# Kernel optimization log

Hardware: AMD Instinct MI355X
Metric: run time of the kernel (lower is better)

The kernel has to match this reference:

```python
import jax, jax.numpy as jnp
import numpy as np

EPS = 1e-6

def _rms_norm(x):
    xf = x.astype(jnp.float32)
    var = jnp.mean(xf * xf, axis=-1, keepdims=True)
    return (xf * jax.lax.rsqrt(var + EPS)).astype(x.dtype)

def setup_inputs() -> dict:
    key = jax.random.key(0)
    k1, k2 = jax.random.split(key)
    B, N, T, D = 16, 768, 48, 2048
    patches = jax.random.normal(k1, (B, N, D), dtype=jnp.float32)
    task_tokens = jax.random.normal(k2, (B, T, D), dtype=jnp.float32)
    task_token_mask = jnp.ones((B, T), dtype=bool)  # True = valid token
    return {"patches": patches, "task_tokens": task_tokens, "task_token_mask": task_token_mask}

def reference(patches, task_tokens, task_token_mask):
    D = patches.shape[-1]
    scale = 1.0 / np.sqrt(D)
    patches_n = _rms_norm(patches)          # [B,N,D]
    task_n = _rms_norm(task_tokens)         # [B,T,D]
    # additive attention bias: 0 for valid task tokens, finfo.min for masked
    neg = jnp.finfo(patches_n.dtype).min
    bias = jnp.where(task_token_mask[:, None, :], 0.0, neg).astype(patches_n.dtype)  # [B,1,T]
    # scaled dot-product attention: patches attend to task tokens
    logits = jnp.einsum('bnd,btd->bnt', patches_n, task_n) * scale + bias
    attn = jax.nn.softmax(logits, axis=-1)
    queries_raw = jnp.einsum('bnt,btd->bnd', attn, task_n)  # [B,N,D]
    queries = _rms_norm(queries_raw)
    # importance score: each query scores every patch
    score = jnp.einsum('bnd,bmd->bnm', queries, patches_n) * scale  # [B,N,N]
    # differentiable selection (select_soft, noise_scale=None):
    # straight-through: hard one-hot of argmax + soft softmax - stop_grad(soft)
    soft = jax.nn.softmax(score, axis=-1)
    hard = jax.nn.one_hot(jnp.argmax(score, axis=-1), score.shape[-1], dtype=score.dtype)
    sel = hard + soft - jax.lax.stop_gradient(soft)
    return sel
```

## Files before the change

kernel.cpp:

```cpp
#include <hip/hip_runtime.h>
#include <math.h>

#define NB 16
#define NN 768
#define NT 48
#define ND 2048
#define NROW (NB*NN)
#define SCALE 0.02209708691207961f
#define NEGBIG (-3.4028234663852886e38f)
#define TAU 2e-3f
#define KS 512
#define MSPLIT 16
#define MCH (NN/MSPLIT)

typedef _Float16 f16;
typedef f16  f16x8 __attribute__((ext_vector_type(8)));
typedef f16  f16x4 __attribute__((ext_vector_type(4)));
typedef float f32x4 __attribute__((ext_vector_type(4)));

__device__ __forceinline__ void stage16(const void* g, void* l) {
    __builtin_amdgcn_global_load_lds(
        (const __attribute__((address_space(1))) unsigned int*)g,
        (__attribute__((address_space(3))) unsigned int*)l, 16, 0, 0);
}

__device__ __forceinline__ void ins4m(float v[4], int idx[4], float nv, int ni) {
    const bool b0 = (v[0] >= nv);
    const bool b1 = (v[1] >= nv);
    const bool b2 = (v[2] >= nv);
    const bool b3 = (v[3] >= nv);
    const int pos = (int)b0 + (int)b1 + (int)b2 + (int)b3;
    if (pos <= 3) { if (pos == 3) { v[3] = nv; idx[3] = ni; } else { v[3] = v[2]; idx[3] = idx[2]; } }
    if (pos <= 2) { if (pos == 2) { v[2] = nv; idx[2] = ni; } else { v[2] = v[1]; idx[2] = idx[1]; } }
    if (pos <= 1) { if (pos == 1) { v[1] = nv; idx[1] = ni; } else { v[1] = v[0]; idx[1] = idx[0]; } }
    if (pos == 0) { v[0] = nv; idx[0] = ni; }
}

__global__ __launch_bounds__(256) void k_prep_task(const float* __restrict__ task,
                                                   float* __restrict__ task_n,
                                                   f16* __restrict__ t_hi,
                                                   f16* __restrict__ t_lo) {
    __shared__ float sred[8];
    const int row = blockIdx.x;
    const float4* src = (const float4*)(task + (size_t)row * ND);
    const int tid = threadIdx.x;
    float4 v0 = src[tid];
    float4 v1 = src[tid + 256];
    float s = v0.x*v0.x + v0.y*v0.y + v0.z*v0.z + v0.w*v0.w
            + v1.x*v1.x + v1.y*v1.y + v1.z*v1.z + v1.w*v1.w;
    #pragma unroll
    for (int off = 32; off > 0; off >>= 1) s += __shfl_down(s, off, 64);
    if ((tid & 63) == 0) sred[tid >> 6] = s;
    __syncthreads();
    if (tid == 0)
        sred[4] = 1.0f / sqrtf((sred[0]+sred[1]+sred[2]+sred[3]) * (1.0f/ND) + 1e-6f);
    __syncthreads();
    const float inv = sred[4];
    const size_t o = (size_t)row * ND;
    f16x4 h0, l0, h1, l1;
    float4 n0, n1;
    #pragma unroll
    for (int e = 0; e < 4; e++) {
        float f0 = (&v0.x)[e] * inv, f1 = (&v1.x)[e] * inv;
        (&n0.x)[e] = f0; (&n1.x)[e] = f1;
        f16 a = (f16)f0; h0[e] = a; l0[e] = (f16)(f0 - (float)a);
        f16 c = (f16)f1; h1[e] = c; l1[e] = (f16)(f1 - (float)c);
    }
    *(float4*)&task_n[o + tid*4]          = n0;
    *(float4*)&task_n[o + (tid+256)*4]    = n1;
    *(f16x4*)&t_hi[o + tid*4]             = h0;
    *(f16x4*)&t_lo[o + tid*4]             = l0;
    *(f16x4*)&t_hi[o + (tid+256)*4]       = h1;
    *(f16x4*)&t_lo[o + (tid+256)*4]       = l1;
}

__global__ __launch_bounds__(256) void k_R(const float* __restrict__ patches,
                                           const f16* __restrict__ t_hi,
                                           const f16* __restrict__ t_lo,
                                           float* __restrict__ Rpart,
                                           float* __restrict__ ssqpart) {
    __shared__ __align__(16) char Ah[64*128], Al[64*128];
    __shared__ __align__(16) char Bh[48*128], Bl[48*128];
    const int rt = blockIdx.x, ks = blockIdx.y, b = blockIdx.z;
    const int tid = threadIdx.x, wid = tid >> 6, lane = tid & 63;
    const int q15 = lane & 15, g4 = lane >> 4;
    const int trow = tid >> 2, tq = tid & 3;
    const int lr = lane >> 3, lgch = (lane & 7) ^ lr;
    const int cxor = q15 & 7;

    const float* gP = patches + ((size_t)(b*NN + rt*64))*ND + ks*KS;
    const f16* gTh = t_hi + (size_t)b*NT*ND + ks*KS;
    const f16* gTl = t_lo + (size_t)b*NT*ND + ks*KS;

    f32x4 acc[3];
    #pragma unroll
    for (int j = 0; j < 3; j++) acc[j] = (f32x4){0.f,0.f,0.f,0.f};
    float ssq = 0.f;

    const float* aptr = gP + (size_t)trow*ND + tq*16;
    float4 va[4], vb[4];
    #pragma unroll
    for (int k = 0; k < 4; k++) va[k] = *(const float4*)(aptr + k*4);

    auto body = [&](float4 (&v)[4], float4 (&vn)[4], int kk, bool last) {
        #pragma unroll
        for (int t2 = 0; t2 < 2; t2++) {
            const int u = wid + 4*t2;
            if (u < 6) {
                stage16(gTh + (size_t)(u*8 + lr)*ND + kk + lgch*8, Bh + u*1024);
                stage16(gTl + (size_t)(u*8 + lr)*ND + kk + lgch*8, Bl + u*1024);
            }
        }
        __builtin_amdgcn_sched_barrier(0);
        if (!last) {
            #pragma unroll
            for (int k = 0; k < 4; k++)
                vn[k] = *(const float4*)(aptr + kk + 64 + k*4);
        }
        __builtin_amdgcn_sched_barrier(0);
        float lssq = 0.f;
        f16x8 hi8[2], lo8[2];
        #pragma unroll
        for (int k = 0; k < 4; k++)
            #pragma unroll
            for (int e = 0; e < 4; e++) {
                const float f = (&v[k].x)[e];
                lssq += f*f;
                const f16 h = (f16)f;
                hi8[k>>1][(k&1)*4 + e] = h;
                lo8[k>>1][(k&1)*4 + e] = (f16)(f - (float)h);
            }
        lssq += __shfl_xor(lssq, 1, 64);
        lssq += __shfl_xor(lssq, 2, 64);
        if (tq == 0) ssq += lssq;
        const int rb = trow * 128;
        #pragma unroll
        for (int c = 0; c < 2; c++) {
            const int ch = (2*tq + c) ^ (trow & 7);
            *(f16x8*)(Ah + rb + ch*16) = hi8[c];
            *(f16x8*)(Al + rb + ch*16) = lo8[c];
        }
        __builtin_amdgcn_sched_barrier(0);
        if (last) asm volatile("s_waitcnt vmcnt(0)" ::: "memory");
        else      asm volatile("s_waitcnt vmcnt(4)" ::: "memory");
        asm volatile("s_waitcnt lgkmcnt(0)" ::: "memory");
        __builtin_amdgcn_s_barrier();
        __builtin_amdgcn_sched_barrier(0);
        #pragma unroll
        for (int ksub = 0; ksub < 2; ksub++) {
            const int chb = ((ksub*4 + g4) ^ cxor) << 4;
            const f16x8 a_h = *(const f16x8*)(Ah + (wid*16 + q15)*128 + chb);
            const f16x8 a_l = *(const f16x8*)(Al + (wid*16 + q15)*128 + chb);
            #pragma unroll
            for (int j = 0; j < 3; j++) {
                const f16x8 b_h = *(const f16x8*)(Bh + (j*16 + q15)*128 + chb);
                const f16x8 b_l = *(const f16x8*)(Bl + (j*16 + q15)*128 + chb);
                acc[j] = __builtin_amdgcn_mfma_f32_16x16x32_f16(a_h, b_h, acc[j], 0, 0, 0);
                acc[j] = __builtin_amdgcn_mfma_f32_16x16x32_f16(a_l, b_h, acc[j], 0, 0, 0);
                acc[j] = __builtin_amdgcn_mfma_f32_16x16x32_f16(a_h, b_l, acc[j], 0, 0, 0);
            }
        }
        asm volatile("" ::: "memory");
        __builtin_amdgcn_s_barrier();
        __builtin_amdgcn_sched_barrier(0);
    };

    body(va, vb,   0, false);
    body(vb, va,  64, false);
    body(va, vb, 128, false);
    body(vb, va, 192, false);
    body(va, vb, 256, false);
    body(vb, va, 320, false);
    body(va, vb, 384, false);
    body(vb, va, 448, true);

    const int grow = b*NN + rt*64;
    #pragma unroll
    for (int j = 0; j < 3; j++)
        #pragma unroll
        for (int r = 0; r < 4; r++)
            Rpart[((size_t)ks*NROW + grow + wid*16 + g4*4 + r)*48 + j*16 + q15] = acc[j][r];
    if (tq == 0)
        ssqpart[(size_t)ks*NROW + grow + trow] = ssq;
}

__global__ __launch_bounds__(256) void k_combine(const float* __restrict__ Rpart,
                                                 const float* __restrict__ ssqpart,
                                                 const int* __restrict__ mask,
                                                 float* __restrict__ R,
                                                 float* __restrict__ w,
                                                 float* __restrict__ pinv) {
    const int r = blockIdx.x * 256 + threadIdx.x;
    const int b = r / NN;
    float ss = 0.f;
    #pragma unroll
    for (int ks = 0; ks < 4; ks++) ss += ssqpart[(size_t)ks*NROW + r];
    const float pv = 1.0f / sqrtf(ss * (1.0f/ND) + 1e-6f);
    pinv[r] = pv;
    float l[48];
    float mx = -INFINITY;
    #pragma unroll
    for (int t4 = 0; t4 < 12; t4++) {
        float4 a = {0.f,0.f,0.f,0.f};
        #pragma unroll
        for (int ks = 0; ks < 4; ks++) {
            const float4 p = *(const float4*)&Rpart[((size_t)ks*NROW + r)*48 + t4*4];
            a.x += p.x; a.y += p.y; a.z += p.z; a.w += p.w;
        }
        *(float4*)&R[(size_t)r*48 + t4*4] = a;
        #pragma unroll
        for (int e = 0; e < 4; e++) {
            const int t = t4*4 + e;
            const float bias = mask[b*NT + t] ? 0.0f : NEGBIG;
            l[t] = (&a.x)[e] * pv * SCALE + bias;
            mx = fmaxf(mx, l[t]);
        }
    }
    float sum = 0.f;
    #pragma unroll
    for (int t = 0; t < 48; t++) { l[t] = expf(l[t] - mx); sum += l[t]; }
    const float inv = 1.0f / sum;
    #pragma unroll
    for (int t4 = 0; t4 < 12; t4++) {
        float4 o;
        #pragma unroll
        for (int e = 0; e < 4; e++) (&o.x)[e] = l[t4*4 + e] * inv;
        *(float4*)&w[(size_t)r*48 + t4*4] = o;
    }
}

__global__ __launch_bounds__(256) void k_scoreW(const float* __restrict__ w,
                                                const float* __restrict__ R,
                                                const float* __restrict__ pinv,
                                                float4* __restrict__ part) {
    __shared__ float Rl[MCH*48];
    __shared__ float pl[MCH];
    const int rt = blockIdx.x, ms = blockIdx.y;
    const int tid = threadIdx.x;
    const int row = rt*256 + tid;
    const int b = row / NN;
    const int m0g = b*NN + ms*MCH;
    for (int u = tid; u < MCH*12; u += 256) {
        const int m = u / 12, t4 = u % 12;
        *(float4*)&Rl[m*48 + t4*4] = *(const float4*)&R[((size_t)(m0g + m))*48 + t4*4];
    }
    if (tid < MCH) pl[tid] = pinv[m0g + tid];
    __syncthreads();
    float4 wr[12];
    #pragma unroll
    for (int t4 = 0; t4 < 12; t4++)
        wr[t4] = *(const float4*)&w[(size_t)row*48 + t4*4];
    float tv[4] = {-INFINITY, -INFINITY, -INFINITY, -INFINITY};
    int   ti[4] = {0x7FFFFFFF, 0x7FFFFFFF, 0x7FFFFFFF, 0x7FFFFFFF};
    #pragma unroll 2
    for (int m = 0; m < MCH; m += 4) {
        float s0 = 0.f, s1 = 0.f, s2 = 0.f, s3 = 0.f;
        #pragma unroll
        for (int t4 = 0; t4 < 12; t4++) {
            const float4 r0 = *(const float4*)&Rl[(m+0)*48 + t4*4];
            const float4 r1 = *(const float4*)&Rl[(m+1)*48 + t4*4];
            const float4 r2 = *(const float4*)&Rl[(m+2)*48 + t4*4];
            const float4 r3 = *(const float4*)&Rl[(m+3)*48 + t4*4];
            const float4 wv = wr[t4];
            s0 = fmaf(wv.x, r0.x, s0); s1 = fmaf(wv.x, r1.x, s1);
            s2 = fmaf(wv.x, r2.x, s2); s3 = fmaf(wv.x, r3.x, s3);
            s0 = fmaf(wv.y, r0.y, s0); s1 = fmaf(wv.y, r1.y, s1);
            s2 = fmaf(wv.y, r2.y, s2); s3 = fmaf(wv.y, r3.y, s3);
            s0 = fmaf(wv.z, r0.z, s0); s1 = fmaf(wv.z, r1.z, s1);
            s2 = fmaf(wv.z, r2.z, s2); s3 = fmaf(wv.z, r3.z, s3);
            s0 = fmaf(wv.w, r0.w, s0); s1 = fmaf(wv.w, r1.w, s1);
            s2 = fmaf(wv.w, r2.w, s2); s3 = fmaf(wv.w, r3.w, s3);
        }
        s0 *= pl[m+0]; s1 *= pl[m+1]; s2 *= pl[m+2]; s3 *= pl[m+3];
        const float gm = fmaxf(fmaxf(s0, s1), fmaxf(s2, s3));
        if (gm >= tv[3]) {
            const int mg = ms*MCH + m;
            ins4m(tv, ti, s0, mg+0);
            ins4m(tv, ti, s1, mg+1);
            ins4m(tv, ti, s2, mg+2);
            ins4m(tv, ti, s3, mg+3);
        }
    }
    part[((size_t)row*MSPLIT + ms)*2]     = make_float4(tv[0], __int_as_float(ti[0]), tv[1], __int_as_float(ti[1]));
    part[((size_t)row*MSPLIT + ms)*2 + 1] = make_float4(tv[2], __int_as_float(ti[2]), tv[3], __int_as_float(ti[3]));
}

__global__ __launch_bounds__(256) void k_final(const float* __restrict__ patches,
                                               const float* __restrict__ task_n,
                                               const float* __restrict__ w,
                                               const float* __restrict__ pinv,
                                               const float4* __restrict__ part,
                                               float* __restrict__ out) {
    __shared__ float qrow[ND];
    __shared__ float wl[48];
    __shared__ int   scand[64];
    __shared__ float swv[4];
    __shared__ int   swi[4];
    __shared__ int   s_idx, s_cnt;
    const int row = blockIdx.x;
    const int b = row / NN;
    const int tid = threadIdx.x, wid = tid >> 6, lane = tid & 63;

    if (wid == 0) {
        const float2 e = ((const float2*)part)[(size_t)row*64 + lane];
        const float myv = e.x;
        const int   myi = __float_as_int(e.y);
        float v = myv; int i = myi;
        #pragma unroll
        for (int off = 1; off <= 32; off <<= 1) {
            const float ov = __shfl_xor(v, off, 64);
            const int   oi = __shfl_xor(i, off, 64);
            if (ov > v || (ov == v && oi < i)) { v = ov; i = oi; }
        }
        const bool in_tau = (myv >= v - TAU);
        const unsigned long long mb  = __ballot(in_tau);
        const unsigned long long mb4 = __ballot(in_tau && ((lane & 3) == 3));
        if (lane == 0) {
            s_idx = i;
            s_cnt = mb4 ? 999 : __popcll(mb);
        }
        if (in_tau) {
            const unsigned long long below = mb & ((lane == 0) ? 0ull : (~0ull >> (64 - lane)));
            scand[__popcll(below)] = myi;
        }
    }
    __syncthreads();
    const int cnt = s_cnt;
    if (cnt > 1) {
        if (tid < 12) *(float4*)&wl[tid*4] = *(const float4*)&w[(size_t)row*48 + tid*4];
        __syncthreads();
        {
            float q[8] = {0.f,0.f,0.f,0.f,0.f,0.f,0.f,0.f};
            for (int t = 0; t < NT; t++) {
                const float wt = wl[t];
                const float* Tn = task_n + ((size_t)(b*NT + t))*ND + tid*8;
                const float4 u0 = *(const float4*)Tn;
                const float4 u1 = *(const float4*)(Tn + 4);
                q[0] = fmaf(wt, u0.x, q[0]); q[1] = fmaf(wt, u0.y, q[1]);
                q[2] = fmaf(wt, u0.z, q[2]); q[3] = fmaf(wt, u0.w, q[3]);
                q[4] = fmaf(wt, u1.x, q[4]); q[5] = fmaf(wt, u1.y, q[5]);
                q[6] = fmaf(wt, u1.z, q[6]); q[7] = fmaf(wt, u1.w, q[7]);
            }
            #pragma unroll
            for (int e2 = 0; e2 < 8; e2++) qrow[tid*8 + e2] = q[e2];
        }
        __syncthreads();
        float bw = -INFINITY; int bi = 0x7FFFFFFF;
        if (cnt != 999) {
            for (int c = wid; c < cnt; c += 4) {
                const int m = scand[c];
                const float* prow = patches + ((size_t)b*NN + m)*ND + lane*32;
                const float* qp = qrow + lane*32;
                float s = 0.f;
                #pragma unroll
                for (int k = 0; k < 8; k++) {
                    const float4 p = *(const float4*)(prow + k*4);
                    const float4 qv = *(const float4*)(qp + k*4);
                    s = fmaf(p.x, qv.x, s); s = fmaf(p.y, qv.y, s);
                    s = fmaf(p.z, qv.z, s); s = fmaf(p.w, qv.w, s);
                }
                #pragma unroll
                for (int off = 32; off > 0; off >>= 1) s += __shfl_down(s, off, 64);
                if (lane == 0) {
                    s *= pinv[b*NN + m];
                    if (s > bw || (s == bw && m < bi)) { bw = s; bi = m; }
                }
            }
        } else {
            for (int m = wid; m < NN; m += 4) {
                const float* prow = patches + ((size_t)b*NN + m)*ND + lane*32;
                const float* qp = qrow + lane*32;
                float s = 0.f;
                #pragma unroll
                for (int k = 0; k < 8; k++) {
                    const float4 p = *(const float4*)(prow + k*4);
                    const float4 qv = *(const float4*)(qp + k*4);
                    s = fmaf(p.x, qv.x, s); s = fmaf(p.y, qv.y, s);
                    s = fmaf(p.z, qv.z, s); s = fmaf(p.w, qv.w, s);
                }
                #pragma unroll
                for (int off = 32; off > 0; off >>= 1) s += __shfl_down(s, off, 64);
                if (lane == 0) {
                    s *= pinv[b*NN + m];
                    if (s > bw || (s == bw && m < bi)) { bw = s; bi = m; }
                }
            }
        }
        if (lane == 0) { swv[wid] = bw; swi[wid] = bi; }
        __syncthreads();
        if (tid == 0) {
            float v = swv[0]; int i = swi[0];
            #pragma unroll
            for (int k = 1; k < 4; k++) {
                if (swv[k] > v || (swv[k] == v && swi[k] < i)) { v = swv[k]; i = swi[k]; }
            }
            s_idx = i;
        }
        __syncthreads();
    }
    const int m = s_idx;
    if (tid < 192) {
        float4 o = {0.f, 0.f, 0.f, 0.f};
        if ((m >> 2) == tid) ((float*)&o)[m & 3] = 1.0f;
        ((float4*)(out + (size_t)row*NN))[tid] = o;
    }
}

extern "C" void kernel_launch(void* const* d_in, const int* in_sizes, int n_in,
                              void* d_out, int out_size, void* d_ws, size_t ws_size,
                              hipStream_t stream) {
    const float* patches = (const float*)d_in[0];
    const float* task    = (const float*)d_in[1];
    const int*   mask    = (const int*)d_in[2];
    float* out = (float*)d_out;

    char* p = (char*)d_ws;
    float* task_n  = (float*)p;  p += (size_t)NB*NT*ND*sizeof(float);
    f16*   t_hi    = (f16*)p;    p += (size_t)NB*NT*ND*sizeof(f16);
    f16*   t_lo    = (f16*)p;    p += (size_t)NB*NT*ND*sizeof(f16);
    float* Rpart   = (float*)p;  p += (size_t)4*NROW*48*sizeof(float);
    float* ssqpart = (float*)p;  p += (size_t)4*NROW*sizeof(float);
    float* R       = (float*)p;  p += (size_t)NROW*48*sizeof(float);
    float* w       = (float*)p;  p += (size_t)NROW*48*sizeof(float);
    float* pinv    = (float*)p;  p += (size_t)NROW*sizeof(float);
    float4* part   = (float4*)p; p += (size_t)NROW*MSPLIT*2*sizeof(float4);

    k_prep_task<<<NB*NT, 256, 0, stream>>>(task, task_n, t_hi, t_lo);
    k_R<<<dim3(NN/64, 4, NB), 256, 0, stream>>>(patches, t_hi, t_lo, Rpart, ssqpart);
    k_combine<<<NROW/256, 256, 0, stream>>>(Rpart, ssqpart, mask, R, w, pinv);
    k_scoreW<<<dim3(NROW/256, MSPLIT), 256, 0, stream>>>(w, R, pinv, part);
    k_final<<<NROW, 256, 0, stream>>>(patches, task_n, w, pinv, part, out);
}
```

Measured before the change: 98.57 us.

## Compute low-rank score matrix with split-f16 MFMA and top-2 candidates

Replaces the scalar FP32 score kernel (w·R with per-thread top-4 insertion) with an MFMA kernel. It uses hi/lo f16 splits of the softmax weights and of the normalized R (three MFMAs per tile), padded to K=64, and keeps top-2 candidates per 64-column chunk via lane shuffles. k_combine now emits the f16 split operands, and k_final reads 24 candidates instead of 64 with a tighter tau. The intent is to move the dominant NxN score work onto matrix cores, at the cost of some precision and fewer candidates for tie detection.

```diff
diff --git a/kernel.cpp b/kernel.cpp
--- a/kernel.cpp
+++ b/kernel.cpp
@@ -8,10 +8,8 @@
 #define NROW (NB*NN)
 #define SCALE 0.02209708691207961f
 #define NEGBIG (-3.4028234663852886e38f)
-#define TAU 2e-3f
+#define TAU 1e-3f
 #define KS 512
-#define MSPLIT 16
-#define MCH (NN/MSPLIT)
 
 typedef _Float16 f16;
 typedef f16  f16x8 __attribute__((ext_vector_type(8)));
@@ -22,18 +20,6 @@
     __builtin_amdgcn_global_load_lds(
         (const __attribute__((address_space(1))) unsigned int*)g,
         (__attribute__((address_space(3))) unsigned int*)l, 16, 0, 0);
-}
-
-__device__ __forceinline__ void ins4m(float v[4], int idx[4], float nv, int ni) {
-    const bool b0 = (v[0] >= nv);
-    const bool b1 = (v[1] >= nv);
-    const bool b2 = (v[2] >= nv);
-    const bool b3 = (v[3] >= nv);
-    const int pos = (int)b0 + (int)b1 + (int)b2 + (int)b3;
-    if (pos <= 3) { if (pos == 3) { v[3] = nv; idx[3] = ni; } else { v[3] = v[2]; idx[3] = idx[2]; } }
-    if (pos <= 2) { if (pos == 2) { v[2] = nv; idx[2] = ni; } else { v[2] = v[1]; idx[2] = idx[1]; } }
-    if (pos <= 1) { if (pos == 1) { v[1] = nv; idx[1] = ni; } else { v[1] = v[0]; idx[1] = idx[0]; } }
-    if (pos == 0) { v[0] = nv; idx[0] = ni; }
 }
 
 __global__ __launch_bounds__(256) void k_prep_task(const float* __restrict__ task,
@@ -187,9 +173,12 @@
 __global__ __launch_bounds__(256) void k_combine(const float* __restrict__ Rpart,
                                                  const float* __restrict__ ssqpart,
                                                  const int* __restrict__ mask,
-                                                 float* __restrict__ R,
                                                  float* __restrict__ w,
-                                                 float* __restrict__ pinv) {
+                                                 float* __restrict__ pinv,
+                                                 f16* __restrict__ Whi,
+                                                 f16* __restrict__ Wlo,
+                                                 f16* __restrict__ Ghi,
+                                                 f16* __restrict__ Glo) {
     const int r = blockIdx.x * 256 + threadIdx.x;
     const int b = r / NN;
     float ss = 0.f;
@@ -207,14 +196,19 @@
             const float4 p = *(const float4*)&Rpart[((size_t)ks*NROW + r)*48 + t4*4];
             a.x += p.x; a.y += p.y; a.z += p.z; a.w += p.w;
         }
-        *(float4*)&R[(size_t)r*48 + t4*4] = a;
+        f16x4 gh, gl;
         #pragma unroll
         for (int e = 0; e < 4; e++) {
+            const float g = (&a.x)[e] * pv;
+            const f16 hh = (f16)g;
+            gh[e] = hh; gl[e] = (f16)(g - (float)hh);
             const int t = t4*4 + e;
             const float bias = mask[b*NT + t] ? 0.0f : NEGBIG;
-            l[t] = (&a.x)[e] * pv * SCALE + bias;
+            l[t] = g * SCALE + bias;
             mx = fmaxf(mx, l[t]);
         }
+        *(f16x4*)&Ghi[(size_t)r*64 + t4*4] = gh;
+        *(f16x4*)&Glo[(size_t)r*64 + t4*4] = gl;
     }
     float sum = 0.f;
     #pragma unroll
@@ -223,66 +217,106 @@
     #pragma unroll
     for (int t4 = 0; t4 < 12; t4++) {
         float4 o;
-        #pragma unroll
-        for (int e = 0; e < 4; e++) (&o.x)[e] = l[t4*4 + e] * inv;
+        f16x4 wh, wlv;
+        #pragma unroll
+        for (int e = 0; e < 4; e++) {
+            const float wv = l[t4*4 + e] * inv;
+            (&o.x)[e] = wv;
+            const f16 hh = (f16)wv;
+            wh[e] = hh; wlv[e] = (f16)(wv - (float)hh);
+        }
         *(float4*)&w[(size_t)r*48 + t4*4] = o;
-    }
-}
-
-__global__ __launch_bounds__(256) void k_scoreW(const float* __restrict__ w,
-                                                const float* __restrict__ R,
-                                                const float* __restrict__ pinv,
+        *(f16x4*)&Whi[(size_t)r*64 + t4*4] = wh;
+        *(f16x4*)&Wlo[(size_t)r*64 + t4*4] = wlv;
+    }
+    const f16x4 z = {(f16)0.f, (f16)0.f, (f16)0.f, (f16)0.f};
+    #pragma unroll
+    for (int t4 = 12; t4 < 16; t4++) {
+        *(f16x4*)&Whi[(size_t)r*64 + t4*4] = z;
+        *(f16x4*)&Wlo[(size_t)r*64 + t4*4] = z;
+        *(f16x4*)&Ghi[(size_t)r*64 + t4*4] = z;
+        *(f16x4*)&Glo[(size_t)r*64 + t4*4] = z;
+    }
+}
+
+__global__ __launch_bounds__(256) void k_scoreM(const f16* __restrict__ Whi,
+                                                const f16* __restrict__ Wlo,
+                                                const f16* __restrict__ Ghi,
+                                                const f16* __restrict__ Glo,
                                                 float4* __restrict__ part) {
-    __shared__ float Rl[MCH*48];
-    __shared__ float pl[MCH];
-    const int rt = blockIdx.x, ms = blockIdx.y;
-    const int tid = threadIdx.x;
-    const int row = rt*256 + tid;
-    const int b = row / NN;
-    const int m0g = b*NN + ms*MCH;
-    for (int u = tid; u < MCH*12; u += 256) {
-        const int m = u / 12, t4 = u % 12;
-        *(float4*)&Rl[m*48 + t4*4] = *(const float4*)&R[((size_t)(m0g + m))*48 + t4*4];
-    }
-    if (tid < MCH) pl[tid] = pinv[m0g + tid];
-    __syncthreads();
-    float4 wr[12];
-    #pragma unroll
-    for (int t4 = 0; t4 < 12; t4++)
-        wr[t4] = *(const float4*)&w[(size_t)row*48 + t4*4];
-    float tv[4] = {-INFINITY, -INFINITY, -INFINITY, -INFINITY};
-    int   ti[4] = {0x7FFFFFFF, 0x7FFFFFFF, 0x7FFFFFFF, 0x7FFFFFFF};
-    #pragma unroll 2
-    for (int m = 0; m < MCH; m += 4) {
-        float s0 = 0.f, s1 = 0.f, s2 = 0.f, s3 = 0.f;
-        #pragma unroll
-        for (int t4 = 0; t4 < 12; t4++) {
-            const float4 r0 = *(const float4*)&Rl[(m+0)*48 + t4*4];
-            const float4 r1 = *(const float4*)&Rl[(m+1)*48 + t4*4];
-            const float4 r2 = *(const float4*)&Rl[(m+2)*48 + t4*4];
-            const float4 r3 = *(const float4*)&Rl[(m+3)*48 + t4*4];
-            const float4 wv = wr[t4];
-            s0 = fmaf(wv.x, r0.x, s0); s1 = fmaf(wv.x, r1.x, s1);
-            s2 = fmaf(wv.x, r2.x, s2); s3 = fmaf(wv.x, r3.x, s3);
-            s0 = fmaf(wv.y, r0.y, s0); s1 = fmaf(wv.y, r1.y, s1);
-            s2 = fmaf(wv.y, r2.y, s2); s3 = fmaf(wv.y, r3.y, s3);
-            s0 = fmaf(wv.z, r0.z, s0); s1 = fmaf(wv.z, r1.z, s1);
-            s2 = fmaf(wv.z, r2.z, s2); s3 = fmaf(wv.z, r3.z, s3);
-            s0 = fmaf(wv.w, r0.w, s0); s1 = fmaf(wv.w, r1.w, s1);
-            s2 = fmaf(wv.w, r2.w, s2); s3 = fmaf(wv.w, r3.w, s3);
-        }
-        s0 *= pl[m+0]; s1 *= pl[m+1]; s2 *= pl[m+2]; s3 *= pl[m+3];
-        const float gm = fmaxf(fmaxf(s0, s1), fmaxf(s2, s3));
-        if (gm >= tv[3]) {
-            const int mg = ms*MCH + m;
-            ins4m(tv, ti, s0, mg+0);
-            ins4m(tv, ti, s1, mg+1);
-            ins4m(tv, ti, s2, mg+2);
-            ins4m(tv, ti, s3, mg+3);
-        }
-    }
-    part[((size_t)row*MSPLIT + ms)*2]     = make_float4(tv[0], __int_as_float(ti[0]), tv[1], __int_as_float(ti[1]));
-    part[((size_t)row*MSPLIT + ms)*2 + 1] = make_float4(tv[2], __int_as_float(ti[2]), tv[3], __int_as_float(ti[3]));
+    const int mt = blockIdx.x, rt = blockIdx.y, b = blockIdx.z;
+    const int tid = threadIdx.x, wid = tid >> 6, lane = tid & 63;
+    const int q15 = lane & 15, g4 = lane >> 4;
+    const int wr = wid >> 1, wc = wid & 1;
+
+    const size_t n0 = (size_t)(b*NN + rt*128 + wr*64);
+    const size_t m0 = (size_t)(b*NN + mt*128 + wc*64);
+    const int mbase = mt*128 + wc*64;
+
+    f16x8 ah[4][2], al[4][2], bh[4][2], bl[4][2];
+    #pragma unroll
+    for (int i = 0; i < 4; i++)
+        #pragma unroll
+        for (int ksub = 0; ksub < 2; ksub++) {
+            const size_t ao = (n0 + i*16 + q15)*64 + ksub*32 + g4*8;
+            ah[i][ksub] = *(const f16x8*)&Whi[ao];
+            al[i][ksub] = *(const f16x8*)&Wlo[ao];
+            const size_t bo = (m0 + i*16 + q15)*64 + ksub*32 + g4*8;
+            bh[i][ksub] = *(const f16x8*)&Ghi[bo];
+            bl[i][ksub] = *(const f16x8*)&Glo[bo];
+        }
+
+    f32x4 acc[4][4];
+    #pragma unroll
+    for (int i = 0; i < 4; i++)
+        #pragma unroll
+        for (int j = 0; j < 4; j++) acc[i][j] = (f32x4){0.f,0.f,0.f,0.f};
+
+    #pragma unroll
+    for (int ksub = 0; ksub < 2; ksub++)
+        #pragma unroll
+        for (int i = 0; i < 4; i++)
+            #pragma unroll
+            for (int j = 0; j < 4; j++) {
+                acc[i][j] = __builtin_amdgcn_mfma_f32_16x16x32_f16(ah[i][ksub], bh[j][ksub], acc[i][j], 0, 0, 0);
+                acc[i][j] = __builtin_amdgcn_mfma_f32_16x16x32_f16(al[i][ksub], bh[j][ksub], acc[i][j], 0, 0, 0);
+                acc[i][j] = __builtin_amdgcn_mfma_f32_16x16x32_f16(ah[i][ksub], bl[j][ksub], acc[i][j], 0, 0, 0);
+            }
+
+    #pragma unroll
+    for (int i = 0; i < 4; i++) {
+        #pragma unroll
+        for (int r = 0; r < 4; r++) {
+            float v1 = -INFINITY, v2 = -INFINITY;
+            int   i1 = 0x7FFFFFFF, i2 = 0x7FFFFFFF;
+            #pragma unroll
+            for (int j = 0; j < 4; j++) {
+                const float s = acc[i][j][r];
+                const int m = mbase + j*16 + q15;
+                if (s > v1) { v2 = v1; i2 = i1; v1 = s; i1 = m; }
+                else if (s > v2) { v2 = s; i2 = m; }
+            }
+            #pragma unroll
+            for (int off = 1; off <= 8; off <<= 1) {
+                const float ov1 = __shfl_xor(v1, off, 64);
+                const int   oi1 = __shfl_xor(i1, off, 64);
+                const float ov2 = __shfl_xor(v2, off, 64);
+                const int   oi2 = __shfl_xor(i2, off, 64);
+                if (ov1 > v1 || (ov1 == v1 && oi1 < i1)) {
+                    if (v1 > ov2 || (v1 == ov2 && i1 < oi2)) { v2 = v1; i2 = i1; }
+                    else { v2 = ov2; i2 = oi2; }
+                    v1 = ov1; i1 = oi1;
+                } else {
+                    if (ov1 > v2 || (ov1 == v2 && oi1 < i2)) { v2 = ov1; i2 = oi1; }
+                }
+            }
+            if (q15 == 0) {
+                const size_t rowg = (size_t)b*NN + rt*128 + wr*64 + i*16 + g4*4 + r;
+                part[rowg*12 + mt*2 + wc] =
+                    make_float4(v1, __int_as_float(i1), v2, __int_as_float(i2));
+            }
+        }
+    }
 }
 
 __global__ __launch_bounds__(256) void k_final(const float* __restrict__ patches,
@@ -293,7 +327,7 @@
                                                float* __restrict__ out) {
     __shared__ float qrow[ND];
     __shared__ float wl[48];
-    __shared__ int   scand[64];
+    __shared__ int   scand[24];
     __shared__ float swv[4];
     __shared__ int   swi[4];
     __shared__ int   s_idx, s_cnt;
@@ -302,9 +336,11 @@
     const int tid = threadIdx.x, wid = tid >> 6, lane = tid & 63;
 
     if (wid == 0) {
-        const float2 e = ((const float2*)part)[(size_t)row*64 + lane];
-        const float myv = e.x;
-        const int   myi = __float_as_int(e.y);
+        float myv = -INFINITY; int myi = 0x7FFFFFFF;
+        if (lane < 24) {
+            const float2 e = ((const float2*)part)[(size_t)row*24 + lane];
+            myv = e.x; myi = __float_as_int(e.y);
+        }
         float v = myv; int i = myi;
         #pragma unroll
         for (int off = 1; off <= 32; off <<= 1) {
@@ -314,12 +350,12 @@
         }
         const bool in_tau = (myv >= v - TAU);
         const unsigned long long mb  = __ballot(in_tau);
-        const unsigned long long mb4 = __ballot(in_tau && ((lane & 3) == 3));
+        const unsigned long long mbr = __ballot(in_tau && ((lane & 1) == 1));
         if (lane == 0) {
             s_idx = i;
-            s_cnt = mb4 ? 999 : __popcll(mb);
-        }
-        if (in_tau) {
+            s_cnt = mbr ? 999 : __popcll(mb);
+        }
+        if (in_tau && lane < 24) {
             const unsigned long long below = mb & ((lane == 0) ? 0ull : (~0ull >> (64 - lane)));
             scand[__popcll(below)] = myi;
         }
@@ -420,14 +456,18 @@
     f16*   t_lo    = (f16*)p;    p += (size_t)NB*NT*ND*sizeof(f16);
     float* Rpart   = (float*)p;  p += (size_t)4*NROW*48*sizeof(float);
     float* ssqpart = (float*)p;  p += (size_t)4*NROW*sizeof(float);
-    float* R       = (float*)p;  p += (size_t)NROW*48*sizeof(float);
     float* w       = (float*)p;  p += (size_t)NROW*48*sizeof(float);
     float* pinv    = (float*)p;  p += (size_t)NROW*sizeof(float);
-    float4* part   = (float4*)p; p += (size_t)NROW*MSPLIT*2*sizeof(float4);
+    f16*   Whi     = (f16*)p;    p += (size_t)NROW*64*sizeof(f16);
+    f16*   Wlo     = (f16*)p;    p += (size_t)NROW*64*sizeof(f16);
+    f16*   Ghi     = (f16*)p;    p += (size_t)NROW*64*sizeof(f16);
+    f16*   Glo     = (f16*)p;    p += (size_t)NROW*64*sizeof(f16);
+    float4* part   = (float4*)p; p += (size_t)NROW*12*sizeof(float4);
 
     k_prep_task<<<NB*NT, 256, 0, stream>>>(task, task_n, t_hi, t_lo);
     k_R<<<dim3(NN/64, 4, NB), 256, 0, stream>>>(patches, t_hi, t_lo, Rpart, ssqpart);
-    k_combine<<<NROW/256, 256, 0, stream>>>(Rpart, ssqpart, mask, R, w, pinv);
-    k_scoreW<<<dim3(NROW/256, MSPLIT), 256, 0, stream>>>(w, R, pinv, part);
+    k_combine<<<NROW/256, 256, 0, stream>>>(Rpart, ssqpart, mask, w, pinv,
+                                            Whi, Wlo, Ghi, Glo);
+    k_scoreM<<<dim3(6, 6, NB), 256, 0, stream>>>(Whi, Wlo, Ghi, Glo, part);
     k_final<<<NROW, 256, 0, stream>>>(patches, task_n, w, pinv, part, out);
 }
```

New measurement: 121.7 us. 23.4% more time.
